# Optimization experiments

Hardware: AMD Instinct MI355X
Metric: run time of the kernel (lower is better)

The kernel has to match this reference:

```python
import jax, jax.numpy as jnp
import numpy as np

DEG2RAD = np.float32(np.pi / 180.0)
RAD2DEG = np.float32(180.0 / np.pi)
TINY = np.float32(1e-6)

# DH table [a, alpha(deg), d, theta_offset(deg)] from the original module
_DH = np.array([[0.0, 180.0, -650.0, 0.0],
                [270.0, 90.0, 0.0, 0.0],
                [800.0, 0.0, 0.0, 0.0],
                [140.0, 90.0, -908.0, 0.0],
                [0.0, -96.0, 0.0, 0.0],
                [0.0, -65.0, 260.0, 0.0]], dtype=np.float32)

BATCH = 1048576


def setup_inputs() -> dict:
    key = jax.random.key(0)
    theta = jax.random.normal(key, (BATCH, 6), dtype=jnp.float32) * 90.0  # joint angles in degrees
    dh = jnp.asarray(_DH)
    return {"theta": theta, "dh": dh}


def _fk(theta, dh):
    B = theta.shape[0]
    th = (dh[None, :, 3] + theta) * DEG2RAD          # [B,6] joint angle in radians
    ct, st = jnp.cos(th), jnp.sin(th)
    al = dh[:, 1] * DEG2RAD                           # [6]
    ca, sa = jnp.cos(al), jnp.sin(al)
    a, d = dh[:, 0], dh[:, 2]
    zeros = jnp.zeros((B,), theta.dtype)
    ones = jnp.ones((B,), theta.dtype)
    T = None
    for i in range(6):  # fixed 6-joint chain (structural, not data dim)
        c, s = ct[:, i], st[:, i]
        r0 = jnp.stack([c, -s, zeros, a[i] * ones], axis=-1)
        r1 = jnp.stack([s * ca[i], c * ca[i], -sa[i] * ones, -sa[i] * d[i] * ones], axis=-1)
        r2 = jnp.stack([s * sa[i], c * sa[i], ca[i] * ones, ca[i] * d[i] * ones], axis=-1)
        r3 = jnp.stack([zeros, zeros, zeros, ones], axis=-1)
        Ti = jnp.stack([r0, r1, r2, r3], axis=1)      # [B,4,4]
        T = Ti if T is None else jnp.einsum('bij,bjk->bik', T, Ti)
    # pose extraction (ZYX-style euler via atan2), branchless via where
    T00, T01, T02 = T[:, 0, 0], T[:, 0, 1], T[:, 0, 2]
    T10, T11, T12 = T[:, 1, 0], T[:, 1, 1], T[:, 1, 2]
    T22 = T[:, 2, 2]
    cond = (jnp.abs(T12) <= TINY) & (jnp.abs(T22) <= TINY)  # gimbal branch
    # branch 1: C=0 => cos(C)=1, so divide_no_nan(x, 1) == x
    A1 = jnp.arctan2(T10, T11) * RAD2DEG
    B1 = jnp.arctan2(T02, T22) * RAD2DEG
    # branch 2
    A2 = jnp.arctan2(-T01, T00) * RAD2DEG
    Ar = A2 * DEG2RAD
    sA, cA = jnp.sin(Ar), jnp.cos(Ar)
    B2 = jnp.arctan2(T02, cA * T00 - sA * T01) * RAD2DEG
    C2 = jnp.arctan2(-T12, T22) * RAD2DEG
    A = jnp.where(cond, A1, A2)
    Bd = jnp.where(cond, B1, B2)
    C = jnp.where(cond, jnp.zeros_like(C2), C2)
    return jnp.stack([T[:, 0, 3], T[:, 1, 3], T[:, 2, 3], A, Bd, C], axis=-1)  # [B,6]


def reference(theta, dh):
    return _fk(theta, dh)
```

## Files before the change

kernel.cpp:

```cpp
#include <hip/hip_runtime.h>
#include <math.h>

#define DEG2RAD 0.017453292519943295f
#define RAD2DEG 57.29577951308232f
#define TINYV   1e-6f

__global__ __launch_bounds__(256) void fk_kernel(const float* __restrict__ theta,
                                                 const float* __restrict__ dh,
                                                 float* __restrict__ out,
                                                 int B) {
    int b = blockIdx.x * blockDim.x + threadIdx.x;
    if (b >= B) return;

    const float* tp = theta + (size_t)b * 6;
    float2 t01 = *(const float2*)(tp + 0);
    float2 t23 = *(const float2*)(tp + 2);
    float2 t45 = *(const float2*)(tp + 4);
    float th[6] = {t01.x, t01.y, t23.x, t23.y, t45.x, t45.y};

    float T[3][4];
    #pragma unroll
    for (int i = 0; i < 6; ++i) {
        float a_  = dh[i*4 + 0];
        float al  = dh[i*4 + 1] * DEG2RAD;
        float d_  = dh[i*4 + 2];
        float off = dh[i*4 + 3];
        float thr = (off + th[i]) * DEG2RAD;
        float s, c, sa, ca;
        __sincosf(thr, &s, &c);
        __sincosf(al,  &sa, &ca);

        if (i == 0) {
            T[0][0] = c;      T[0][1] = -s;     T[0][2] = 0.f;  T[0][3] = a_;
            T[1][0] = s * ca; T[1][1] = c * ca; T[1][2] = -sa;  T[1][3] = -sa * d_;
            T[2][0] = s * sa; T[2][1] = c * sa; T[2][2] = ca;   T[2][3] = ca * d_;
        } else {
            float sca = s * ca, cca = c * ca, ssa = s * sa, csa = c * sa;
            float nsd = -sa * d_, cad = ca * d_;
            #pragma unroll
            for (int r = 0; r < 3; ++r) {
                float t0 = T[r][0], t1 = T[r][1], t2 = T[r][2], t3 = T[r][3];
                T[r][0] = t0 * c   + t1 * sca + t2 * ssa;
                T[r][1] = -t0 * s  + t1 * cca + t2 * csa;
                T[r][2] =           -t1 * sa  + t2 * ca;
                T[r][3] = t0 * a_  + t1 * nsd + t2 * cad + t3;
            }
        }
    }

    float T00 = T[0][0], T01 = T[0][1], T02 = T[0][2];
    float T10 = T[1][0], T11 = T[1][1], T12 = T[1][2];
    float T22 = T[2][2];

    bool cond = (fabsf(T12) <= TINYV) && (fabsf(T22) <= TINYV);

    float A1 = atan2f(T10, T11) * RAD2DEG;
    float B1 = atan2f(T02, T22) * RAD2DEG;
    float A2 = atan2f(-T01, T00) * RAD2DEG;
    float Ar = A2 * DEG2RAD;
    float sA, cA;
    __sincosf(Ar, &sA, &cA);
    float B2 = atan2f(T02, cA * T00 - sA * T01) * RAD2DEG;
    float C2 = atan2f(-T12, T22) * RAD2DEG;

    float A  = cond ? A1 : A2;
    float Bd = cond ? B1 : B2;
    float C  = cond ? 0.f : C2;

    float* op = out + (size_t)b * 6;
    float2 o0 = {T[0][3], T[1][3]};
    float2 o1 = {T[2][3], A};
    float2 o2 = {Bd, C};
    *(float2*)(op + 0) = o0;
    *(float2*)(op + 2) = o1;
    *(float2*)(op + 4) = o2;
}

extern "C" void kernel_launch(void* const* d_in, const int* in_sizes, int n_in,
                              void* d_out, int out_size, void* d_ws, size_t ws_size,
                              hipStream_t stream) {
    const float* theta = (const float*)d_in[0];
    const float* dh    = (const float*)d_in[1];
    float* out = (float*)d_out;
    int B = in_sizes[0] / 6;
    int block = 256;
    int grid = (B + block - 1) / block;
    fk_kernel<<<grid, block, 0, stream>>>(theta, dh, out, B);
}
```

Before: 85.35 us.

## Process two rows per thread with fast sincos, polynomial atan2 and skipped gimbal branch

```diff
diff --git a/kernel.cpp b/kernel.cpp
--- a/kernel.cpp
+++ b/kernel.cpp
@@ -1,79 +1,116 @@
 #include <hip/hip_runtime.h>
 #include <math.h>
 
-#define DEG2RAD 0.017453292519943295f
 #define RAD2DEG 57.29577951308232f
+#define INV360  (1.0f/360.0f)
 #define TINYV   1e-6f
+
+__device__ __forceinline__ void sincos_rev(float rev, float* s, float* c) {
+    float r = rev - floorf(rev);
+    *s = __builtin_amdgcn_sinf(r);
+    *c = __builtin_amdgcn_cosf(r);
+}
+
+__device__ __forceinline__ float fast_atan2f(float y, float x) {
+    float ax = fabsf(x), ay = fabsf(y);
+    float mx = fmaxf(ax, ay), mn = fminf(ax, ay);
+    float q = mn * __builtin_amdgcn_rcpf(mx);
+    q = (mx == 0.0f) ? 0.0f : q;
+    float s = q * q;
+    float p =        -0.0117212f;
+    p = fmaf(p, s,  0.05265332f);
+    p = fmaf(p, s, -0.11643287f);
+    p = fmaf(p, s,  0.19354346f);
+    p = fmaf(p, s, -0.33262347f);
+    p = fmaf(p, s,  0.99997726f);
+    float r = p * q;
+    r = (ay > ax)  ? (1.57079632679f - r) : r;
+    r = (x < 0.0f) ? (3.14159265359f - r) : r;
+    return copysignf(r, y);
+}
 
 __global__ __launch_bounds__(256) void fk_kernel(const float* __restrict__ theta,
                                                  const float* __restrict__ dh,
                                                  float* __restrict__ out,
-                                                 int B) {
-    int b = blockIdx.x * blockDim.x + threadIdx.x;
-    if (b >= B) return;
+                                                 int Bpairs) {
+    int p = blockIdx.x * blockDim.x + threadIdx.x;
+    if (p >= Bpairs) return;
 
-    const float* tp = theta + (size_t)b * 6;
-    float2 t01 = *(const float2*)(tp + 0);
-    float2 t23 = *(const float2*)(tp + 2);
-    float2 t45 = *(const float2*)(tp + 4);
-    float th[6] = {t01.x, t01.y, t23.x, t23.y, t45.x, t45.y};
+    const float4* tp = (const float4*)(theta + (size_t)p * 12);
+    float4 f0 = tp[0];
+    float4 f1 = tp[1];
+    float4 f2 = tp[2];
 
-    float T[3][4];
+    float a_[6], sa[6], ca[6], sad[6], cad[6], offr[6];
     #pragma unroll
     for (int i = 0; i < 6; ++i) {
-        float a_  = dh[i*4 + 0];
-        float al  = dh[i*4 + 1] * DEG2RAD;
-        float d_  = dh[i*4 + 2];
-        float off = dh[i*4 + 3];
-        float thr = (off + th[i]) * DEG2RAD;
-        float s, c, sa, ca;
-        __sincosf(thr, &s, &c);
-        __sincosf(al,  &sa, &ca);
-
-        if (i == 0) {
-            T[0][0] = c;      T[0][1] = -s;     T[0][2] = 0.f;  T[0][3] = a_;
-            T[1][0] = s * ca; T[1][1] = c * ca; T[1][2] = -sa;  T[1][3] = -sa * d_;
-            T[2][0] = s * sa; T[2][1] = c * sa; T[2][2] = ca;   T[2][3] = ca * d_;
-        } else {
-            float sca = s * ca, cca = c * ca, ssa = s * sa, csa = c * sa;
-            float nsd = -sa * d_, cad = ca * d_;
-            #pragma unroll
-            for (int r = 0; r < 3; ++r) {
-                float t0 = T[r][0], t1 = T[r][1], t2 = T[r][2], t3 = T[r][3];
-                T[r][0] = t0 * c   + t1 * sca + t2 * ssa;
-                T[r][1] = -t0 * s  + t1 * cca + t2 * csa;
-                T[r][2] =           -t1 * sa  + t2 * ca;
-                T[r][3] = t0 * a_  + t1 * nsd + t2 * cad + t3;
-            }
-        }
+        a_[i]   = dh[i*4+0];
+        float d = dh[i*4+2];
+        offr[i] = dh[i*4+3] * INV360;
+        float sA, cA;
+        sincos_rev(dh[i*4+1] * INV360, &sA, &cA);
+        sa[i] = sA; ca[i] = cA;
+        sad[i] = -sA * d;
+        cad[i] =  cA * d;
     }
 
-    float T00 = T[0][0], T01 = T[0][1], T02 = T[0][2];
-    float T10 = T[1][0], T11 = T[1][1], T12 = T[1][2];
-    float T22 = T[2][2];
+    float th[2][6] = {{f0.x, f0.y, f0.z, f0.w, f1.x, f1.y},
+                      {f1.z, f1.w, f2.x, f2.y, f2.z, f2.w}};
+    float res[2][6];
 
-    bool cond = (fabsf(T12) <= TINYV) && (fabsf(T22) <= TINYV);
+    #pragma unroll
+    for (int rr = 0; rr < 2; ++rr) {
+        float T00,T01,T02,T03, T10,T11,T12,T13, T20,T21,T22,T23;
+        {
+            float s, c;
+            sincos_rev(fmaf(th[rr][0], INV360, offr[0]), &s, &c);
+            T00 = c;         T01 = -s;         T02 = 0.f;     T03 = a_[0];
+            T10 = s * ca[0]; T11 = c * ca[0];  T12 = -sa[0];  T13 = sad[0];
+            T20 = s * sa[0]; T21 = c * sa[0];  T22 = ca[0];   T23 = cad[0];
+        }
+        #pragma unroll
+        for (int i = 1; i < 6; ++i) {
+            float s, c;
+            sincos_rev(fmaf(th[rr][i], INV360, offr[i]), &s, &c);
+            float sca = s * ca[i], cca = c * ca[i];
+            float ssa = s * sa[i], csa = c * sa[i];
+            float n0, n1, n2, n3;
+            n0 =  T00*c + T01*sca + T02*ssa;
+            n1 = -T00*s + T01*cca + T02*csa;
+            n2 =          -T01*sa[i] + T02*ca[i];
+            n3 =  T00*a_[i] + T01*sad[i] + T02*cad[i] + T03;
+            T00=n0; T01=n1; T02=n2; T03=n3;
+            n0 =  T10*c + T11*sca + T12*ssa;
+            n1 = -T10*s + T11*cca + T12*csa;
+            n2 =          -T11*sa[i] + T12*ca[i];
+            n3 =  T10*a_[i] + T11*sad[i] + T12*cad[i] + T13;
+            T10=n0; T11=n1; T12=n2; T13=n3;
+            n0 =  T20*c + T21*sca + T22*ssa;
+            n1 = -T20*s + T21*cca + T22*csa;
+            n2 =          -T21*sa[i] + T22*ca[i];
+            n3 =  T20*a_[i] + T21*sad[i] + T22*cad[i] + T23;
+            T20=n0; T21=n1; T22=n2; T23=n3;
+        }
 
-    float A1 = atan2f(T10, T11) * RAD2DEG;
-    float B1 = atan2f(T02, T22) * RAD2DEG;
-    float A2 = atan2f(-T01, T00) * RAD2DEG;
-    float Ar = A2 * DEG2RAD;
-    float sA, cA;
-    __sincosf(Ar, &sA, &cA);
-    float B2 = atan2f(T02, cA * T00 - sA * T01) * RAD2DEG;
-    float C2 = atan2f(-T12, T22) * RAD2DEG;
+        bool cond = (fabsf(T12) <= TINYV) && (fabsf(T22) <= TINYV);
+        float A  = fast_atan2f(-T01, T00) * RAD2DEG;
+        float Bd = fast_atan2f(T02, __builtin_amdgcn_sqrtf(fmaf(T00,T00,T01*T01))) * RAD2DEG;
+        float C  = fast_atan2f(-T12, T22) * RAD2DEG;
+        if (__ballot(cond)) {
+            float A1 = fast_atan2f(T10, T11) * RAD2DEG;
+            float B1 = fast_atan2f(T02, T22) * RAD2DEG;
+            A  = cond ? A1  : A;
+            Bd = cond ? B1  : Bd;
+            C  = cond ? 0.f : C;
+        }
+        res[rr][0] = T03; res[rr][1] = T13; res[rr][2] = T23;
+        res[rr][3] = A;   res[rr][4] = Bd;  res[rr][5] = C;
+    }
 
-    float A  = cond ? A1 : A2;
-    float Bd = cond ? B1 : B2;
-    float C  = cond ? 0.f : C2;
-
-    float* op = out + (size_t)b * 6;
-    float2 o0 = {T[0][3], T[1][3]};
-    float2 o1 = {T[2][3], A};
-    float2 o2 = {Bd, C};
-    *(float2*)(op + 0) = o0;
-    *(float2*)(op + 2) = o1;
-    *(float2*)(op + 4) = o2;
+    float4* op = (float4*)(out + (size_t)p * 12);
+    op[0] = make_float4(res[0][0], res[0][1], res[0][2], res[0][3]);
+    op[1] = make_float4(res[0][4], res[0][5], res[1][0], res[1][1]);
+    op[2] = make_float4(res[1][2], res[1][3], res[1][4], res[1][5]);
 }
 
 extern "C" void kernel_launch(void* const* d_in, const int* in_sizes, int n_in,
@@ -82,8 +119,8 @@
     const float* theta = (const float*)d_in[0];
     const float* dh    = (const float*)d_in[1];
     float* out = (float*)d_out;
-    int B = in_sizes[0] / 6;
+    int Bpairs = in_sizes[0] / 12;
     int block = 256;
-    int grid = (B + block - 1) / block;
-    fk_kernel<<<grid, block, 0, stream>>>(theta, dh, out, B);
+    int grid = (Bpairs + block - 1) / block;
+    fk_kernel<<<grid, block, 0, stream>>>(theta, dh, out, Bpairs);
 }
```

After: 83.65 us, median of 2. 1.02x faster.
